# Kernel tuning notes

Hardware: AMD Instinct MI355X
Metric: run time of the kernel (lower is better)

The kernel has to match this reference:

```python
import jax, jax.numpy as jnp
import numpy as np

N = 65536            # query points (256x256 image)
G = 2048             # number of gaussian/gabor primitives
K = 8                # top-k wave frequencies per primitive
NUM_TOTAL_FREQ = 128
MAX_FREQ = 128.0


def setup_inputs() -> dict:
    key = jax.random.key(0)
    ks = jax.random.split(key, 7)
    x = jax.random.uniform(ks[0], (N, 2), jnp.float32)
    gaussian_colors = 0.05 * jax.random.normal(ks[1], (G, 3), jnp.float32)
    gaussian_positions = jax.random.uniform(ks[2], (G, 2), jnp.float32)
    gaussian_scales = 3.0 + 0.05 * jax.random.normal(ks[3], (G, 2), jnp.float32)
    gaussian_rotations = jnp.pi * jax.random.uniform(ks[4], (G, 1), jnp.float32)
    topk_wave_coefficients = 0.01 * (2.0 * jax.random.uniform(ks[5], (G, K), jnp.float32) - 1.0)
    topk_wave_indices = jax.random.randint(ks[6], (G, K), 0, NUM_TOTAL_FREQ)
    return {
        "x": x,
        "gaussian_colors": gaussian_colors,
        "gaussian_positions": gaussian_positions,
        "gaussian_scales": gaussian_scales,
        "gaussian_rotations": gaussian_rotations,
        "topk_wave_coefficients": topk_wave_coefficients,
        "topk_wave_indices": topk_wave_indices,
    }


def reference(x, gaussian_colors, gaussian_positions, gaussian_scales,
              gaussian_rotations, topk_wave_coefficients, topk_wave_indices):
    # Dense (unblocked) faithful evaluation of the periodic-primitive splat:
    # out[n] = sum_g color_g * exp(-0.5*((rx*sx)^2+(ry*sy)^2)) * sum_k c_gk*cos(2*pi*f_gk*rx)
    dx = x[:, None, 0] - gaussian_positions[None, :, 0]   # [N, G]
    dy = x[:, None, 1] - gaussian_positions[None, :, 1]   # [N, G]
    th = gaussian_rotations[:, 0]                          # [G]
    c, s = jnp.cos(th), jnp.sin(th)
    rx = c[None, :] * dx + s[None, :] * dy                 # rotated coords [N, G]
    ry = -s[None, :] * dx + c[None, :] * dy
    sx = gaussian_scales[None, :, 0]
    sy = gaussian_scales[None, :, 1]
    env = jnp.exp(-0.5 * ((rx * sx) ** 2 + (ry * sy) ** 2))  # gaussian envelope [N, G]
    # frequency of each selected coefficient: idx * max_freq / num_total_freq
    freqs = topk_wave_indices.astype(jnp.float32) * (MAX_FREQ / NUM_TOTAL_FREQ)  # [G, K]
    two_pi = 2.0 * jnp.pi
    wave = jnp.zeros_like(env)
    for k in range(K):  # small fixed loop -> avoids materializing [N, G, K]
        wave = wave + topk_wave_coefficients[:, k][None, :] * jnp.cos(two_pi * freqs[:, k][None, :] * rx)
    return (env * wave) @ gaussian_colors  # [N, 3]
```

## Files before the change

kernel.cpp:

```cpp
#include <hip/hip_runtime.h>
#include <math.h>

#define G_NUM   2048
#define N_PTS   65536
#define K_FREQ  8
#define REC     32
#define CHUNKS  16
#define G_PER_CHUNK (G_NUM / CHUNKS)
#define PACK_BYTES ((size_t)G_NUM * REC * sizeof(float))
#define PART_FLOATS ((size_t)N_PTS * 3)
#define PART_BYTES  (PART_FLOATS * sizeof(float) * CHUNKS)

typedef float v2f __attribute__((ext_vector_type(2)));

#if __has_builtin(__builtin_amdgcn_cosf)
__device__ __forceinline__ float hw_cos_rev(float p) { return __builtin_amdgcn_cosf(p); }
#else
__device__ __forceinline__ float hw_cos_rev(float p) { return __cosf(6.28318530717958648f * p); }
#endif
#if __has_builtin(__builtin_amdgcn_exp2f)
__device__ __forceinline__ float hw_exp2(float p) { return __builtin_amdgcn_exp2f(p); }
#else
__device__ __forceinline__ float hw_exp2(float p) { return exp2f(p); }
#endif

__device__ __forceinline__ v2f fma2(v2f a, float b, v2f c) {
#if __has_builtin(__builtin_elementwise_fma)
    v2f bb = {b, b};
    return __builtin_elementwise_fma(a, bb, c);
#else
    v2f r; r.x = fmaf(a.x, b, c.x); r.y = fmaf(a.y, b, c.y); return r;
#endif
}
__device__ __forceinline__ v2f fma2v(v2f a, v2f b, v2f c) {
#if __has_builtin(__builtin_elementwise_fma)
    return __builtin_elementwise_fma(a, b, c);
#else
    v2f r; r.x = fmaf(a.x, b.x, c.x); r.y = fmaf(a.y, b.y, c.y); return r;
#endif
}
__device__ __forceinline__ v2f spread(float b) { v2f r = {b, b}; return r; }

__global__ __launch_bounds__(256) void pack_kernel(
    const float* __restrict__ colors, const float* __restrict__ pos,
    const float* __restrict__ scales, const float* __restrict__ rot,
    const float* __restrict__ coef,   const int* __restrict__ idx,
    float* __restrict__ pack)
{
    int j = blockIdx.x * blockDim.x + threadIdx.x;
    if (j >= G_NUM) return;
    float th = rot[j];
    float c = cosf(th), s = sinf(th);
    float px = pos[2 * j], py = pos[2 * j + 1];
    float sx = scales[2 * j], sy = scales[2 * j + 1];
    const float nhl2e = -0.72134752044448170368f;
    float* r = pack + (size_t)j * REC;
    r[0] = c;
    r[1] = s;
    r[2] = -s;
    r[3] = -(c * px + s * py);
    r[4] = s * px - c * py;
    r[5] = nhl2e * sx * sx;
    r[6] = nhl2e * sy * sy;
    r[7] = colors[3 * j];
    r[8] = colors[3 * j + 1];
    r[9] = colors[3 * j + 2];
#pragma unroll
    for (int k = 0; k < K_FREQ; ++k) {
        r[10 + k] = (float)idx[j * K_FREQ + k];
        r[18 + k] = coef[j * K_FREQ + k];
    }
#pragma unroll
    for (int t = 26; t < REC; ++t) r[t] = 0.0f;
}

template <bool USE_PART>
__global__ __launch_bounds__(256, 4) void periodic2d_kernel(
    const float* __restrict__ x, const float* __restrict__ pack,
    float* __restrict__ dst )
{
    const int t = blockIdx.x * 256 + threadIdx.x;
    const int p0 = t;
    const int p1 = t + N_PTS / 4;
    const int p2 = t + N_PTS / 2;
    const int p3 = t + 3 * (N_PTS / 4);
    const float2 q0 = ((const float2*)x)[p0];
    const float2 q1 = ((const float2*)x)[p1];
    const float2 q2 = ((const float2*)x)[p2];
    const float2 q3 = ((const float2*)x)[p3];
    const v2f xiA = {q0.x, q1.x}, yiA = {q0.y, q1.y};
    const v2f xiB = {q2.x, q3.x}, yiB = {q2.y, q3.y};
    v2f a0A = {0.f, 0.f}, a1A = {0.f, 0.f}, a2A = {0.f, 0.f};
    v2f a0B = {0.f, 0.f}, a1B = {0.f, 0.f}, a2B = {0.f, 0.f};
    const float* __restrict__ r = pack + (size_t)(blockIdx.y * G_PER_CHUNK) * REC;
#pragma unroll 2
    for (int j = 0; j < G_PER_CHUNK; ++j, r += REC) {
        const float cth = r[0], sth = r[1], nsth = r[2];
        const float tx = r[3], ty = r[4], A = r[5], B = r[6];
        const v2f rxA = fma2(xiA, cth, fma2(yiA, sth, spread(tx)));
        const v2f rxB = fma2(xiB, cth, fma2(yiB, sth, spread(tx)));
        const v2f ryA = fma2(yiA, cth, fma2(xiA, nsth, spread(ty)));
        const v2f ryB = fma2(yiB, cth, fma2(xiB, nsth, spread(ty)));
        const v2f eargA = fma2v(ryA * B, ryA, (rxA * A) * rxA);
        const v2f eargB = fma2v(ryB * B, ryB, (rxB * A) * rxB);
        v2f envA, envB;
        envA.x = hw_exp2(eargA.x); envA.y = hw_exp2(eargA.y);
        envB.x = hw_exp2(eargB.x); envB.y = hw_exp2(eargB.y);
        v2f waveA = {0.f, 0.f}, waveB = {0.f, 0.f};
#pragma unroll
        for (int k = 0; k < K_FREQ; ++k) {
            const float fk = r[10 + k], ck = r[18 + k];
            const v2f phA = rxA * fk;
            const v2f phB = rxB * fk;
            v2f cA, cB;
            cA.x = hw_cos_rev(phA.x); cA.y = hw_cos_rev(phA.y);
            cB.x = hw_cos_rev(phB.x); cB.y = hw_cos_rev(phB.y);
            waveA = fma2(cA, ck, waveA);
            waveB = fma2(cB, ck, waveB);
        }
        const v2f wA = envA * waveA;
        const v2f wB = envB * waveB;
        a0A = fma2(wA, r[7], a0A);  a0B = fma2(wB, r[7], a0B);
        a1A = fma2(wA, r[8], a1A);  a1B = fma2(wB, r[8], a1B);
        a2A = fma2(wA, r[9], a2A);  a2B = fma2(wB, r[9], a2B);
    }
    if (USE_PART) {
        float* o = dst + (size_t)blockIdx.y * PART_FLOATS;
        o[3 * p0 + 0] = a0A.x; o[3 * p0 + 1] = a1A.x; o[3 * p0 + 2] = a2A.x;
        o[3 * p1 + 0] = a0A.y; o[3 * p1 + 1] = a1A.y; o[3 * p1 + 2] = a2A.y;
        o[3 * p2 + 0] = a0B.x; o[3 * p2 + 1] = a1B.x; o[3 * p2 + 2] = a2B.x;
        o[3 * p3 + 0] = a0B.y; o[3 * p3 + 1] = a1B.y; o[3 * p3 + 2] = a2B.y;
    } else {
        atomicAdd(&dst[3 * p0 + 0], a0A.x);
        atomicAdd(&dst[3 * p0 + 1], a1A.x);
        atomicAdd(&dst[3 * p0 + 2], a2A.x);
        atomicAdd(&dst[3 * p1 + 0], a0A.y);
        atomicAdd(&dst[3 * p1 + 1], a1A.y);
        atomicAdd(&dst[3 * p1 + 2], a2A.y);
        atomicAdd(&dst[3 * p2 + 0], a0B.x);
        atomicAdd(&dst[3 * p2 + 1], a1B.x);
        atomicAdd(&dst[3 * p2 + 2], a2B.x);
        atomicAdd(&dst[3 * p3 + 0], a0B.y);
        atomicAdd(&dst[3 * p3 + 1], a1B.y);
        atomicAdd(&dst[3 * p3 + 2], a2B.y);
    }
}

__global__ __launch_bounds__(256) void reduce_kernel(
    const float* __restrict__ part, float* __restrict__ out)
{
    const int i = blockIdx.x * 256 + threadIdx.x;
    float4 s = {0.f, 0.f, 0.f, 0.f};
#pragma unroll
    for (int c = 0; c < CHUNKS; ++c) {
        const float4 v = ((const float4*)(part + (size_t)c * PART_FLOATS))[i];
        s.x += v.x; s.y += v.y; s.z += v.z; s.w += v.w;
    }
    ((float4*)out)[i] = s;
}

extern "C" void kernel_launch(void* const* d_in, const int* in_sizes, int n_in,
                              void* d_out, int out_size, void* d_ws, size_t ws_size,
                              hipStream_t stream)
{
    const float* x      = (const float*)d_in[0];
    const float* colors = (const float*)d_in[1];
    const float* pos    = (const float*)d_in[2];
    const float* scales = (const float*)d_in[3];
    const float* rot    = (const float*)d_in[4];
    const float* coef   = (const float*)d_in[5];
    const int*   idx    = (const int*)d_in[6];
    float* out  = (float*)d_out;
    float* pack = (float*)d_ws;
    float* part = (float*)((char*)d_ws + PACK_BYTES);

    pack_kernel<<<dim3((G_NUM + 255) / 256), 256, 0, stream>>>(
        colors, pos, scales, rot, coef, idx, pack);

    if (ws_size >= PACK_BYTES + PART_BYTES) {
        periodic2d_kernel<true><<<dim3(N_PTS / 1024, CHUNKS), 256, 0, stream>>>(
            x, pack, part);
        reduce_kernel<<<dim3((N_PTS * 3 / 4) / 256), 256, 0, stream>>>(part, out);
    } else {
        (void)hipMemsetAsync(d_out, 0, (size_t)out_size * sizeof(float), stream);
        periodic2d_kernel<false><<<dim3(N_PTS / 1024, CHUNKS), 256, 0, stream>>>(
            x, pack, out);
    }
}
```

Baseline: 203.0 us.

## Pre-splat packed parameters as float pairs and double chunk count

The packed per-primitive record now stores every parameter twice, as an adjacent pair. The inner loop can then load v2f operands directly for packed FMAs without broadcasting scalars, and it computes dx/dy by subtraction instead of using precomputed translations. The number of G chunks doubles to 32, the occupancy hint rises to 8 waves, and unrolling is disabled. The costs are twice as much parameter traffic, a partial buffer twice as large that the reduce kernel must read, and possible register pressure under the tighter launch bound.

```diff
diff --git a/kernel.cpp b/kernel.cpp
--- a/kernel.cpp
+++ b/kernel.cpp
@@ -4,8 +4,8 @@
 #define G_NUM   2048
 #define N_PTS   65536
 #define K_FREQ  8
-#define REC     32
-#define CHUNKS  16
+#define REC     64
+#define CHUNKS  32
 #define G_PER_CHUNK (G_NUM / CHUNKS)
 #define PACK_BYTES ((size_t)G_NUM * REC * sizeof(float))
 #define PART_FLOATS ((size_t)N_PTS * 3)
@@ -24,14 +24,6 @@
 __device__ __forceinline__ float hw_exp2(float p) { return exp2f(p); }
 #endif
 
-__device__ __forceinline__ v2f fma2(v2f a, float b, v2f c) {
-#if __has_builtin(__builtin_elementwise_fma)
-    v2f bb = {b, b};
-    return __builtin_elementwise_fma(a, bb, c);
-#else
-    v2f r; r.x = fmaf(a.x, b, c.x); r.y = fmaf(a.y, b, c.y); return r;
-#endif
-}
 __device__ __forceinline__ v2f fma2v(v2f a, v2f b, v2f c) {
 #if __has_builtin(__builtin_elementwise_fma)
     return __builtin_elementwise_fma(a, b, c);
@@ -39,7 +31,6 @@
     v2f r; r.x = fmaf(a.x, b.x, c.x); r.y = fmaf(a.y, b.y, c.y); return r;
 #endif
 }
-__device__ __forceinline__ v2f spread(float b) { v2f r = {b, b}; return r; }
 
 __global__ __launch_bounds__(256) void pack_kernel(
     const float* __restrict__ colors, const float* __restrict__ pos,
@@ -51,31 +42,31 @@
     if (j >= G_NUM) return;
     float th = rot[j];
     float c = cosf(th), s = sinf(th);
-    float px = pos[2 * j], py = pos[2 * j + 1];
     float sx = scales[2 * j], sy = scales[2 * j + 1];
     const float nhl2e = -0.72134752044448170368f;
     float* r = pack + (size_t)j * REC;
-    r[0] = c;
-    r[1] = s;
-    r[2] = -s;
-    r[3] = -(c * px + s * py);
-    r[4] = s * px - c * py;
-    r[5] = nhl2e * sx * sx;
-    r[6] = nhl2e * sy * sy;
-    r[7] = colors[3 * j];
-    r[8] = colors[3 * j + 1];
-    r[9] = colors[3 * j + 2];
+    auto put = [&](int pair, float v) { r[2 * pair] = v; r[2 * pair + 1] = v; };
+    put(0, pos[2 * j]);
+    put(1, pos[2 * j + 1]);
+    put(2, c);
+    put(3, s);
+    put(4, -s);
+    put(5, nhl2e * sx * sx);
+    put(6, nhl2e * sy * sy);
+    put(7, colors[3 * j]);
+    put(8, colors[3 * j + 1]);
+    put(9, colors[3 * j + 2]);
 #pragma unroll
     for (int k = 0; k < K_FREQ; ++k) {
-        r[10 + k] = (float)idx[j * K_FREQ + k];
-        r[18 + k] = coef[j * K_FREQ + k];
+        put(10 + k, (float)idx[j * K_FREQ + k]);
+        put(18 + k, coef[j * K_FREQ + k]);
     }
 #pragma unroll
-    for (int t = 26; t < REC; ++t) r[t] = 0.0f;
+    for (int p = 26; p < 32; ++p) put(p, 0.0f);
 }
 
 template <bool USE_PART>
-__global__ __launch_bounds__(256, 4) void periodic2d_kernel(
+__global__ __launch_bounds__(256, 8) void periodic2d_kernel(
     const float* __restrict__ x, const float* __restrict__ pack,
     float* __restrict__ dst )
 {
@@ -92,38 +83,42 @@
     const v2f xiB = {q2.x, q3.x}, yiB = {q2.y, q3.y};
     v2f a0A = {0.f, 0.f}, a1A = {0.f, 0.f}, a2A = {0.f, 0.f};
     v2f a0B = {0.f, 0.f}, a1B = {0.f, 0.f}, a2B = {0.f, 0.f};
-    const float* __restrict__ r = pack + (size_t)(blockIdx.y * G_PER_CHUNK) * REC;
-#pragma unroll 2
-    for (int j = 0; j < G_PER_CHUNK; ++j, r += REC) {
-        const float cth = r[0], sth = r[1], nsth = r[2];
-        const float tx = r[3], ty = r[4], A = r[5], B = r[6];
-        const v2f rxA = fma2(xiA, cth, fma2(yiA, sth, spread(tx)));
-        const v2f rxB = fma2(xiB, cth, fma2(yiB, sth, spread(tx)));
-        const v2f ryA = fma2(yiA, cth, fma2(xiA, nsth, spread(ty)));
-        const v2f ryB = fma2(yiB, cth, fma2(xiB, nsth, spread(ty)));
-        const v2f eargA = fma2v(ryA * B, ryA, (rxA * A) * rxA);
-        const v2f eargB = fma2v(ryB * B, ryB, (rxB * A) * rxB);
+
+    const v2f* __restrict__ rv =
+        (const v2f*)(pack + (size_t)(blockIdx.y * G_PER_CHUNK) * REC);
+#pragma unroll 1
+    for (int j = 0; j < G_PER_CHUNK; ++j, rv += REC / 2) {
+        const v2f dxA = xiA - rv[0];
+        const v2f dyA = yiA - rv[1];
+        const v2f dxB = xiB - rv[0];
+        const v2f dyB = yiB - rv[1];
+        const v2f rxA = fma2v(dxA, rv[2], dyA * rv[3]);
+        const v2f rxB = fma2v(dxB, rv[2], dyB * rv[3]);
+        const v2f ryA = fma2v(dxA, rv[4], dyA * rv[2]);
+        const v2f ryB = fma2v(dxB, rv[4], dyB * rv[2]);
+        const v2f eargA = fma2v(ryA * rv[6], ryA, (rxA * rv[5]) * rxA);
+        const v2f eargB = fma2v(ryB * rv[6], ryB, (rxB * rv[5]) * rxB);
         v2f envA, envB;
         envA.x = hw_exp2(eargA.x); envA.y = hw_exp2(eargA.y);
         envB.x = hw_exp2(eargB.x); envB.y = hw_exp2(eargB.y);
         v2f waveA = {0.f, 0.f}, waveB = {0.f, 0.f};
 #pragma unroll
         for (int k = 0; k < K_FREQ; ++k) {
-            const float fk = r[10 + k], ck = r[18 + k];
-            const v2f phA = rxA * fk;
-            const v2f phB = rxB * fk;
+            const v2f phA = rxA * rv[10 + k];
+            const v2f phB = rxB * rv[10 + k];
             v2f cA, cB;
             cA.x = hw_cos_rev(phA.x); cA.y = hw_cos_rev(phA.y);
             cB.x = hw_cos_rev(phB.x); cB.y = hw_cos_rev(phB.y);
-            waveA = fma2(cA, ck, waveA);
-            waveB = fma2(cB, ck, waveB);
+            waveA = fma2v(cA, rv[18 + k], waveA);
+            waveB = fma2v(cB, rv[18 + k], waveB);
         }
         const v2f wA = envA * waveA;
         const v2f wB = envB * waveB;
-        a0A = fma2(wA, r[7], a0A);  a0B = fma2(wB, r[7], a0B);
-        a1A = fma2(wA, r[8], a1A);  a1B = fma2(wB, r[8], a1B);
-        a2A = fma2(wA, r[9], a2A);  a2B = fma2(wB, r[9], a2B);
+        a0A = fma2v(wA, rv[7], a0A);  a0B = fma2v(wB, rv[7], a0B);
+        a1A = fma2v(wA, rv[8], a1A);  a1B = fma2v(wB, rv[8], a1B);
+        a2A = fma2v(wA, rv[9], a2A);  a2B = fma2v(wB, rv[9], a2B);
     }
+
     if (USE_PART) {
         float* o = dst + (size_t)blockIdx.y * PART_FLOATS;
         o[3 * p0 + 0] = a0A.x; o[3 * p0 + 1] = a1A.x; o[3 * p0 + 2] = a2A.x;
```

Measured after the change: 204.6 us. No clear change (+0.8%).
